# Kernel optimization log

Hardware: AMD Instinct MI355X
Metric: run time of the kernel (lower is better)

The kernel has to match this reference:

```python
import jax, jax.numpy as jnp
import numpy as np

EMBED_DIM = 1024
NUM_HEADS = 16
HEAD_DIM = EMBED_DIM // NUM_HEADS


def setup_inputs() -> dict:
    key = jax.random.key(0)
    ks = jax.random.split(key, 11)
    B, S, E = 4, 2048, EMBED_DIM
    s = 1.0 / np.sqrt(E)
    return {
        "q": jax.random.normal(ks[0], (B, S, E), jnp.float32),
        "k": jax.random.normal(ks[1], (B, S, E), jnp.float32),
        "v": jax.random.normal(ks[2], (B, S, E), jnp.float32),
        "Wq": jax.random.uniform(ks[3], (E, E), jnp.float32, -s, s),
        "bq": jax.random.uniform(ks[4], (E,), jnp.float32, -s, s),
        "Wk": jax.random.uniform(ks[5], (E, E), jnp.float32, -s, s),
        "bk": jax.random.uniform(ks[6], (E,), jnp.float32, -s, s),
        "Wv": jax.random.uniform(ks[7], (E, E), jnp.float32, -s, s),
        "bv": jax.random.uniform(ks[8], (E,), jnp.float32, -s, s),
        "Wo": jax.random.uniform(ks[9], (E, E), jnp.float32, -s, s),
        "bo": jax.random.uniform(ks[10], (E,), jnp.float32, -s, s),
    }


def _split_heads(x):
    B, S, E = x.shape
    return x.reshape(B, S, NUM_HEADS, HEAD_DIM).transpose(0, 2, 1, 3)  # [B,H,S,D]


def reference(q, k, v, Wq, bq, Wk, bk, Wv, bv, Wo, bo):
    # torch Linear: x @ W.T + b
    Q = _split_heads(q @ Wq.T + bq)
    K = _split_heads(k @ Wk.T + bk)
    V = _split_heads(v @ Wv.T + bv)
    scale = 1.0 / jnp.sqrt(jnp.float32(HEAD_DIM))
    scores = jnp.einsum("bhqd,bhkd->bhqk", Q, K) * scale  # [B,H,S,S]
    weights = jax.nn.softmax(scores, axis=-1)
    ctx = jnp.einsum("bhqk,bhkd->bhqd", weights, V)
    B, H, S, D = ctx.shape
    merged = ctx.transpose(0, 2, 1, 3).reshape(B, S, H * D)
    out = merged @ Wo.T + bo
    return out, weights
```

## Files before the change

### kernel.cpp

```cpp
#include <hip/hip_runtime.h>
#include <hip/hip_bf16.h>

typedef __bf16 bf16x8 __attribute__((ext_vector_type(8)));
typedef float f32x4 __attribute__((ext_vector_type(4)));

constexpr size_t XQ_OFF = 0;
constexpr size_t WQ_OFF = 25165824;
constexpr size_t Q_OFF  = 29360128;
constexpr size_t KK_OFF = 37748736;
constexpr size_t VT_OFF = 46137344;
constexpr size_t CTX_OFF= 54525952;

__device__ __forceinline__ void gload16(const void* g, void* s) {
    __builtin_amdgcn_global_load_lds((__attribute__((address_space(1))) void*)g,
                                     (__attribute__((address_space(3))) void*)s, 16, 0, 0);
}
#define WAIT_VM0()   asm volatile("s_waitcnt vmcnt(0)" ::: "memory")
#define WAIT_VM4()   asm volatile("s_waitcnt vmcnt(4)" ::: "memory")
#define WAIT_VM32()  asm volatile("s_waitcnt vmcnt(32)" ::: "memory")
#define WAIT_LGKM0() asm volatile("s_waitcnt lgkmcnt(0)" ::: "memory")
#define BAR()        __builtin_amdgcn_s_barrier()

__global__ __launch_bounds__(256) void convert_k(
    const float* __restrict__ q, const float* __restrict__ k, const float* __restrict__ v,
    const float* __restrict__ Wq, const float* __restrict__ Wk, const float* __restrict__ Wv,
    const float* __restrict__ Wo, __bf16* __restrict__ ws) {
    int id = blockIdx.x * 256 + threadIdx.x;
    const int NX = 1048576;
    const int NW = 131072;
    const float* src; size_t dst; int local;
    if (id < 3 * NX) {
        int z = id / NX; local = id - z * NX;
        src = (z == 0) ? q : ((z == 1) ? k : v);
        dst = XQ_OFF + (size_t)z * 8388608;
    } else {
        int i2 = id - 3 * NX;
        int z = i2 / NW; local = i2 - z * NW;
        src = (z == 0) ? Wq : ((z == 1) ? Wk : ((z == 2) ? Wv : Wo));
        dst = WQ_OFF + (size_t)z * 1048576;
    }
    const float4* s4 = (const float4*)(src + (size_t)local * 8);
    float4 a = s4[0], b = s4[1];
    bf16x8 o;
    o[0]=(__bf16)a.x; o[1]=(__bf16)a.y; o[2]=(__bf16)a.z; o[3]=(__bf16)a.w;
    o[4]=(__bf16)b.x; o[5]=(__bf16)b.y; o[6]=(__bf16)b.z; o[7]=(__bf16)b.w;
    *(bf16x8*)(ws + dst + (size_t)local * 8) = o;
}

template<int MODE>
__global__ __launch_bounds__(256) void gemm_k(
    __bf16* __restrict__ ws,
    const float* __restrict__ bq, const float* __restrict__ bk,
    const float* __restrict__ bv, const float* __restrict__ bo,
    float* __restrict__ out) {
    const int K = 1024;
    unsigned n = blockIdx.x + 64u * (blockIdx.y + 8u * blockIdx.z);
    unsigned cpx = (MODE == 0) ? 192u : 64u;
    unsigned m_ = (n & 7u) * cpx + (n >> 3);
    unsigned bx = m_ & 63u;
    unsigned rest = m_ >> 6;
    unsigned by = rest & 7u;
    unsigned bz = rest >> 3;

    int z = (int)bz;
    const __bf16* A; const __bf16* Bm; const float* bias;
    if (MODE == 0) {
        A    = ws + XQ_OFF + (size_t)z * 8388608;
        Bm   = ws + WQ_OFF + (size_t)z * 1048576;
        bias = (z == 0) ? bq : ((z == 1) ? bk : bv);
    } else {
        A    = ws + CTX_OFF;
        Bm   = ws + WQ_OFF + (size_t)3 * 1048576;
        bias = bo;
    }
    int row0 = (int)bx * 128, col0 = (int)by * 128;
    __shared__ __align__(16) __bf16 As[2][128 * 32];
    __shared__ __align__(16) __bf16 Bs[2][128 * 32];
    int t = threadIdx.x, lane = t & 63, w = t >> 6;
    int wr = w >> 1, wc = w & 1;
    f32x4 acc[4][4];
#pragma unroll
    for (int i = 0; i < 4; ++i)
#pragma unroll
        for (int j = 0; j < 4; ++j) acc[i][j] = (f32x4){0.f, 0.f, 0.f, 0.f};

    auto stage = [&](int buf, int kt) {
#pragma unroll
        for (int i = 0; i < 2; ++i) {
            int e = ((i * 4 + w) * 64 + lane) * 8;
            int r = e >> 5, c = e & 31;
            gload16(A  + (size_t)(row0 + r) * K + kt + c, &As[buf][e]);
            gload16(Bm + (size_t)(col0 + r) * K + kt + c, &Bs[buf][e]);
        }
    };

    stage(0, 0);
    int cur = 0;
    for (int kt = 0; kt < K; kt += 32) {
        bool nx = kt + 32 < K;
        if (nx) { stage(cur ^ 1, kt + 32); WAIT_VM4(); }
        else    { WAIT_VM0(); }
        BAR();
        const __bf16* Ac = As[cur];
        const __bf16* Bc = Bs[cur];
        bf16x8 af[4], bfr[4];
#pragma unroll
        for (int f = 0; f < 4; ++f) {
            af[f]  = *(const bf16x8*)&Ac[(wr * 64 + f * 16 + (lane & 15)) * 32 + (lane >> 4) * 8];
            bfr[f] = *(const bf16x8*)&Bc[(wc * 64 + f * 16 + (lane & 15)) * 32 + (lane >> 4) * 8];
        }
#pragma unroll
        for (int fr = 0; fr < 4; ++fr)
#pragma unroll
            for (int fc = 0; fc < 4; ++fc)
                acc[fr][fc] = __builtin_amdgcn_mfma_f32_16x16x32_bf16(af[fr], bfr[fc], acc[fr][fc], 0, 0, 0);
        WAIT_LGKM0();
        BAR();
        cur ^= 1;
    }

    if (MODE == 0) {
        __bf16* dqk = ws + Q_OFF + (size_t)z * 8388608;
        __bf16* dvt = ws + VT_OFF;
#pragma unroll
        for (int fr = 0; fr < 4; ++fr)
#pragma unroll
            for (int fc = 0; fc < 4; ++fc)
#pragma unroll
                for (int r = 0; r < 4; ++r) {
                    int m = row0 + wr * 64 + fr * 16 + ((lane >> 4) << 2) + r;
                    int nn = col0 + wc * 64 + fc * 16 + (lane & 15);
                    float val = acc[fr][fc][r] + bias[nn];
                    int bb = m >> 11, s = m & 2047, h = nn >> 6, d = nn & 63;
                    size_t bh = (size_t)bb * 16 + h;
                    if (z < 2) dqk[bh * 131072 + (size_t)s * 64 + d] = (__bf16)val;
                    else       dvt[bh * 131072 + (size_t)d * 2048 + s] = (__bf16)val;
                }
    } else {
#pragma unroll
        for (int fr = 0; fr < 4; ++fr)
#pragma unroll
            for (int fc = 0; fc < 4; ++fc)
#pragma unroll
                for (int r = 0; r < 4; ++r) {
                    int m = row0 + wr * 64 + fr * 16 + ((lane >> 4) << 2) + r;
                    int nn = col0 + wc * 64 + fc * 16 + (lane & 15);
                    out[(size_t)m * 1024 + nn] = acc[fr][fc][r] + bias[nn];
                }
    }
}

__global__ __launch_bounds__(512) void rowsum_k(const __bf16* __restrict__ ws,
                                                float* __restrict__ rs_out) {
    unsigned n = blockIdx.x + 8u * blockIdx.y;
    unsigned m = (n & 7u) * 64u + (n >> 3);
    int bh = (int)(m >> 3);
    int q0 = (int)(m & 7u) * 256;
    const __bf16* Qb = ws + Q_OFF  + (size_t)bh * 131072;
    const __bf16* Kb = ws + KK_OFF + (size_t)bh * 131072;
    __shared__ __align__(16) __bf16 Ks[2][64 * 64];
    int t = threadIdx.x, lane = t & 63, w = t >> 6, g = lane >> 4;
    const float SCALE = 0.125f;

    bf16x8 aq[2][2];
#pragma unroll
    for (int f = 0; f < 2; ++f) {
        int qr = q0 + w * 32 + f * 16 + (lane & 15);
        aq[f][0] = *(const bf16x8*)&Qb[(size_t)qr * 64 + g * 8];
        aq[f][1] = *(const bf16x8*)&Qb[(size_t)qr * 64 + 32 + g * 8];
    }

    { int r = t >> 3, c8 = t & 7;
      gload16(Kb + (size_t)r * 64 + ((c8 ^ (r & 7)) << 3), &Ks[0][t * 8]); }
    WAIT_VM0(); BAR();

    float rs[8] = {0.f,0.f,0.f,0.f,0.f,0.f,0.f,0.f};
    int cur = 0;
    for (int kt = 0; kt < 2048; kt += 64) {
        bool nx = kt < 1984;
        if (nx) {
            int r = t >> 3, c8 = t & 7;
            gload16(Kb + (size_t)(kt + 64 + r) * 64 + ((c8 ^ (r & 7)) << 3), &Ks[cur ^ 1][t * 8]);
        }
        const __bf16* Kc = Ks[cur];
        __builtin_amdgcn_s_setprio(1);
#pragma unroll
        for (int kc = 0; kc < 4; ++kc) {
            int krow = kc * 16 + (lane & 15);
            bf16x8 b0 = *(const bf16x8*)((const char*)Kc + krow * 128 + ((g * 16) ^ ((krow & 7) << 4)));
            bf16x8 b1 = *(const bf16x8*)((const char*)Kc + krow * 128 + (((4 + g) * 16) ^ ((krow & 7) << 4)));
#pragma unroll
            for (int f = 0; f < 2; ++f) {
                f32x4 s = (f32x4){0.f, 0.f, 0.f, 0.f};
                s = __builtin_amdgcn_mfma_f32_16x16x32_bf16(aq[f][0], b0, s, 0, 0, 0);
                s = __builtin_amdgcn_mfma_f32_16x16x32_bf16(aq[f][1], b1, s, 0, 0, 0);
#pragma unroll
                for (int r4 = 0; r4 < 4; ++r4) rs[f * 4 + r4] += __expf(s[r4] * SCALE);
            }
        }
        __builtin_amdgcn_s_setprio(0);
        WAIT_LGKM0();
        if (nx) WAIT_VM0();
        BAR();
        cur ^= 1;
    }
#pragma unroll
    for (int msk = 1; msk < 16; msk <<= 1)
#pragma unroll
        for (int i = 0; i < 8; ++i) rs[i] += __shfl_xor(rs[i], msk);
    if ((lane & 15) == 0) {
#pragma unroll
        for (int f = 0; f < 2; ++f)
#pragma unroll
            for (int r4 = 0; r4 < 4; ++r4)
                rs_out[(size_t)bh * 2048 + q0 + w * 32 + f * 16 + g * 4 + r4] = rs[f * 4 + r4];
    }
}

__global__ __launch_bounds__(512) void attnw_k(const __bf16* __restrict__ ws,
                                               const float* __restrict__ rsf,
                                               __bf16* __restrict__ wsw,
                                               float* __restrict__ wout) {
    unsigned n = blockIdx.x + 8u * blockIdx.y;
    unsigned m = (n & 7u) * 64u + (n >> 3);
    int bh = (int)(m >> 3);
    int q0 = (int)(m & 7u) * 256;

    const __bf16* Qb = ws + Q_OFF  + (size_t)bh * 131072;
    const __bf16* Kb = ws + KK_OFF + (size_t)bh * 131072;
    const __bf16* Vb = ws + VT_OFF + (size_t)bh * 131072;
    __bf16* ctx = wsw + CTX_OFF;

    int t = threadIdx.x, lane = t & 63, w = t >> 6, g = lane >> 4;
    __shared__ __align__(16) __bf16 Ps[256 * 64];
    __shared__ __align__(16) __bf16 Ks[2][64 * 64];
    __shared__ __align__(16) __bf16 Vts[2][64 * 64];
    const float SCALE = 0.125f;

    float rinv[8];
#pragma unroll
    for (int f = 0; f < 2; ++f)
#pragma unroll
        for (int r4 = 0; r4 < 4; ++r4)
            rinv[f * 4 + r4] = 1.f / rsf[(size_t)bh * 2048 + q0 + w * 32 + f * 16 + g * 4 + r4];

    bf16x8 aq[2][2];
#pragma unroll
    for (int f = 0; f < 2; ++f) {
        int qr = q0 + w * 32 + f * 16 + (lane & 15);
        aq[f][0] = *(const bf16x8*)&Qb[(size_t)qr * 64 + g * 8];
        aq[f][1] = *(const bf16x8*)&Qb[(size_t)qr * 64 + 32 + g * 8];
    }

    { int r = t >> 3, c8 = t & 7;
      gload16(Kb + (size_t)r * 64   + ((c8 ^ (r & 7)) << 3), &Ks[0][t * 8]);
      gload16(Vb + (size_t)r * 2048 + ((c8 ^ (r & 7)) << 3), &Vts[0][t * 8]); }
    WAIT_VM0(); BAR();

    f32x4 cacc[2][4];
#pragma unroll
    for (int f = 0; f < 2; ++f)
#pragma unroll
        for (int dc = 0; dc < 4; ++dc) cacc[f][dc] = (f32x4){0.f, 0.f, 0.f, 0.f};

    int cur = 0;
    for (int kt = 0; kt < 2048; kt += 64) {
        bool nx = kt < 1984;
        if (nx) {
            int r = t >> 3, c8 = t & 7;
            gload16(Kb + (size_t)(kt + 64 + r) * 64 + ((c8 ^ (r & 7)) << 3), &Ks[cur ^ 1][t * 8]);
            gload16(Vb + (size_t)r * 2048 + (kt + 64) + ((c8 ^ (r & 7)) << 3), &Vts[cur ^ 1][t * 8]);
        }
        const __bf16* Kc = Ks[cur];
        const __bf16* Vc = Vts[cur];
        __builtin_amdgcn_s_setprio(1);
#pragma unroll
        for (int kc = 0; kc < 4; ++kc) {
            int krow = kc * 16 + (lane & 15);
            bf16x8 b0 = *(const bf16x8*)((const char*)Kc + krow * 128 + ((g * 16) ^ ((krow & 7) << 4)));
            bf16x8 b1 = *(const bf16x8*)((const char*)Kc + krow * 128 + (((4 + g) * 16) ^ ((krow & 7) << 4)));
#pragma unroll
            for (int f = 0; f < 2; ++f) {
                f32x4 s = (f32x4){0.f, 0.f, 0.f, 0.f};
                s = __builtin_amdgcn_mfma_f32_16x16x32_bf16(aq[f][0], b0, s, 0, 0, 0);
                s = __builtin_amdgcn_mfma_f32_16x16x32_bf16(aq[f][1], b1, s, 0, 0, 0);
                size_t wbase = ((size_t)bh * 2048 + q0 + w * 32 + f * 16 + (g << 2)) * 2048
                               + kt + kc * 16 + (lane & 15);
#pragma unroll
                for (int r4 = 0; r4 < 4; ++r4) {
                    float e = __expf(s[r4] * SCALE) * rinv[f * 4 + r4];
                    wout[wbase + (size_t)r4 * 2048] = e;
                    int prow = w * 32 + f * 16 + (g << 2) + r4;
                    int pcol = kc * 16 + (lane & 15);
                    *(__bf16*)((char*)Ps + prow * 128 + ((pcol * 2) ^ ((prow & 7) << 4))) = (__bf16)e;
                }
            }
        }
        __builtin_amdgcn_s_setprio(0);
        WAIT_LGKM0();
        __builtin_amdgcn_sched_barrier(0);
        BAR();
        __builtin_amdgcn_s_setprio(1);
#pragma unroll
        for (int ks = 0; ks < 2; ++ks) {
            bf16x8 ap[2];
#pragma unroll
            for (int f = 0; f < 2; ++f) {
                int arow = w * 32 + f * 16 + (lane & 15);
                ap[f] = *(const bf16x8*)((const char*)Ps + arow * 128 + ((ks * 64 + g * 16) ^ ((arow & 7) << 4)));
            }
#pragma unroll
            for (int dc = 0; dc < 4; ++dc) {
                int vrow = dc * 16 + (lane & 15);
                bf16x8 bv = *(const bf16x8*)((const char*)Vc + vrow * 128 + ((ks * 64 + g * 16) ^ ((vrow & 7) << 4)));
#pragma unroll
                for (int f = 0; f < 2; ++f)
                    cacc[f][dc] = __builtin_amdgcn_mfma_f32_16x16x32_bf16(ap[f], bv, cacc[f][dc], 0, 0, 0);
            }
        }
        __builtin_amdgcn_s_setprio(0);
        WAIT_LGKM0();
        WAIT_VM32();
        BAR();
        cur ^= 1;
    }

    int bb = bh >> 4, h = bh & 15;
#pragma unroll
    for (int f = 0; f < 2; ++f)
#pragma unroll
        for (int dc = 0; dc < 4; ++dc)
#pragma unroll
            for (int r4 = 0; r4 < 4; ++r4) {
                int qg = q0 + w * 32 + f * 16 + (g << 2) + r4;
                int d = dc * 16 + (lane & 15);
                ctx[((size_t)bb * 2048 + qg) * 1024 + h * 64 + d] = (__bf16)cacc[f][dc][r4];
            }
}

extern "C" void kernel_launch(void* const* d_in, const int* in_sizes, int n_in,
                              void* d_out, int out_size, void* d_ws, size_t ws_size,
                              hipStream_t stream) {
    const float* q  = (const float*)d_in[0];
    const float* k  = (const float*)d_in[1];
    const float* v  = (const float*)d_in[2];
    const float* Wq = (const float*)d_in[3];
    const float* bq = (const float*)d_in[4];
    const float* Wk = (const float*)d_in[5];
    const float* bk = (const float*)d_in[6];
    const float* Wv = (const float*)d_in[7];
    const float* bv = (const float*)d_in[8];
    const float* Wo = (const float*)d_in[9];
    const float* bo = (const float*)d_in[10];
    __bf16* ws = (__bf16*)d_ws;
    float* out  = (float*)d_out;
    float* wout = out + 8388608;
    float* rsum = (float*)d_ws;

    convert_k<<<dim3(14336), dim3(256), 0, stream>>>(q, k, v, Wq, Wk, Wv, Wo, ws);
    gemm_k<0><<<dim3(64, 8, 3), dim3(256), 0, stream>>>(ws, bq, bk, bv, bo, out);
    rowsum_k<<<dim3(8, 64), dim3(512), 0, stream>>>(ws, rsum);
    attnw_k<<<dim3(8, 64), dim3(512), 0, stream>>>(ws, rsum, ws, wout);
    gemm_k<1><<<dim3(64, 8, 1), dim3(256), 0, stream>>>(ws, bq, bk, bv, bo, out);
}
```

Before: 558.1 us.

## Fuse rowsum into PV kernel and move weights write to separate kernel

```diff
diff --git a/kernel.cpp b/kernel.cpp
--- a/kernel.cpp
+++ b/kernel.cpp
@@ -17,7 +17,6 @@
 }
 #define WAIT_VM0()   asm volatile("s_waitcnt vmcnt(0)" ::: "memory")
 #define WAIT_VM4()   asm volatile("s_waitcnt vmcnt(4)" ::: "memory")
-#define WAIT_VM32()  asm volatile("s_waitcnt vmcnt(32)" ::: "memory")
 #define WAIT_LGKM0() asm volatile("s_waitcnt lgkmcnt(0)" ::: "memory")
 #define BAR()        __builtin_amdgcn_s_barrier()
 
@@ -150,77 +149,9 @@
     }
 }
 
-__global__ __launch_bounds__(512) void rowsum_k(const __bf16* __restrict__ ws,
-                                                float* __restrict__ rs_out) {
-    unsigned n = blockIdx.x + 8u * blockIdx.y;
-    unsigned m = (n & 7u) * 64u + (n >> 3);
-    int bh = (int)(m >> 3);
-    int q0 = (int)(m & 7u) * 256;
-    const __bf16* Qb = ws + Q_OFF  + (size_t)bh * 131072;
-    const __bf16* Kb = ws + KK_OFF + (size_t)bh * 131072;
-    __shared__ __align__(16) __bf16 Ks[2][64 * 64];
-    int t = threadIdx.x, lane = t & 63, w = t >> 6, g = lane >> 4;
-    const float SCALE = 0.125f;
-
-    bf16x8 aq[2][2];
-#pragma unroll
-    for (int f = 0; f < 2; ++f) {
-        int qr = q0 + w * 32 + f * 16 + (lane & 15);
-        aq[f][0] = *(const bf16x8*)&Qb[(size_t)qr * 64 + g * 8];
-        aq[f][1] = *(const bf16x8*)&Qb[(size_t)qr * 64 + 32 + g * 8];
-    }
-
-    { int r = t >> 3, c8 = t & 7;
-      gload16(Kb + (size_t)r * 64 + ((c8 ^ (r & 7)) << 3), &Ks[0][t * 8]); }
-    WAIT_VM0(); BAR();
-
-    float rs[8] = {0.f,0.f,0.f,0.f,0.f,0.f,0.f,0.f};
-    int cur = 0;
-    for (int kt = 0; kt < 2048; kt += 64) {
-        bool nx = kt < 1984;
-        if (nx) {
-            int r = t >> 3, c8 = t & 7;
-            gload16(Kb + (size_t)(kt + 64 + r) * 64 + ((c8 ^ (r & 7)) << 3), &Ks[cur ^ 1][t * 8]);
-        }
-        const __bf16* Kc = Ks[cur];
-        __builtin_amdgcn_s_setprio(1);
-#pragma unroll
-        for (int kc = 0; kc < 4; ++kc) {
-            int krow = kc * 16 + (lane & 15);
-            bf16x8 b0 = *(const bf16x8*)((const char*)Kc + krow * 128 + ((g * 16) ^ ((krow & 7) << 4)));
-            bf16x8 b1 = *(const bf16x8*)((const char*)Kc + krow * 128 + (((4 + g) * 16) ^ ((krow & 7) << 4)));
-#pragma unroll
-            for (int f = 0; f < 2; ++f) {
-                f32x4 s = (f32x4){0.f, 0.f, 0.f, 0.f};
-                s = __builtin_amdgcn_mfma_f32_16x16x32_bf16(aq[f][0], b0, s, 0, 0, 0);
-                s = __builtin_amdgcn_mfma_f32_16x16x32_bf16(aq[f][1], b1, s, 0, 0, 0);
-#pragma unroll
-                for (int r4 = 0; r4 < 4; ++r4) rs[f * 4 + r4] += __expf(s[r4] * SCALE);
-            }
-        }
-        __builtin_amdgcn_s_setprio(0);
-        WAIT_LGKM0();
-        if (nx) WAIT_VM0();
-        BAR();
-        cur ^= 1;
-    }
-#pragma unroll
-    for (int msk = 1; msk < 16; msk <<= 1)
-#pragma unroll
-        for (int i = 0; i < 8; ++i) rs[i] += __shfl_xor(rs[i], msk);
-    if ((lane & 15) == 0) {
-#pragma unroll
-        for (int f = 0; f < 2; ++f)
-#pragma unroll
-            for (int r4 = 0; r4 < 4; ++r4)
-                rs_out[(size_t)bh * 2048 + q0 + w * 32 + f * 16 + g * 4 + r4] = rs[f * 4 + r4];
-    }
-}
-
-__global__ __launch_bounds__(512) void attnw_k(const __bf16* __restrict__ ws,
-                                               const float* __restrict__ rsf,
-                                               __bf16* __restrict__ wsw,
-                                               float* __restrict__ wout) {
+__global__ __launch_bounds__(512) void softpv_k(const __bf16* __restrict__ ws,
+                                                float* __restrict__ rs_out,
+                                                __bf16* __restrict__ wsw) {
     unsigned n = blockIdx.x + 8u * blockIdx.y;
     unsigned m = (n & 7u) * 64u + (n >> 3);
     int bh = (int)(m >> 3);
@@ -237,13 +168,6 @@
     __shared__ __align__(16) __bf16 Vts[2][64 * 64];
     const float SCALE = 0.125f;
 
-    float rinv[8];
-#pragma unroll
-    for (int f = 0; f < 2; ++f)
-#pragma unroll
-        for (int r4 = 0; r4 < 4; ++r4)
-            rinv[f * 4 + r4] = 1.f / rsf[(size_t)bh * 2048 + q0 + w * 32 + f * 16 + g * 4 + r4];
-
     bf16x8 aq[2][2];
 #pragma unroll
     for (int f = 0; f < 2; ++f) {
@@ -262,6 +186,7 @@
     for (int f = 0; f < 2; ++f)
 #pragma unroll
         for (int dc = 0; dc < 4; ++dc) cacc[f][dc] = (f32x4){0.f, 0.f, 0.f, 0.f};
+    float rs[8] = {0.f,0.f,0.f,0.f,0.f,0.f,0.f,0.f};
 
     int cur = 0;
     for (int kt = 0; kt < 2048; kt += 64) {
@@ -284,12 +209,10 @@
                 f32x4 s = (f32x4){0.f, 0.f, 0.f, 0.f};
                 s = __builtin_amdgcn_mfma_f32_16x16x32_bf16(aq[f][0], b0, s, 0, 0, 0);
                 s = __builtin_amdgcn_mfma_f32_16x16x32_bf16(aq[f][1], b1, s, 0, 0, 0);
-                size_t wbase = ((size_t)bh * 2048 + q0 + w * 32 + f * 16 + (g << 2)) * 2048
-                               + kt + kc * 16 + (lane & 15);
 #pragma unroll
                 for (int r4 = 0; r4 < 4; ++r4) {
-                    float e = __expf(s[r4] * SCALE) * rinv[f * 4 + r4];
-                    wout[wbase + (size_t)r4 * 2048] = e;
+                    float e = __expf(s[r4] * SCALE);
+                    rs[f * 4 + r4] += e;
                     int prow = w * 32 + f * 16 + (g << 2) + r4;
                     int pcol = kc * 16 + (lane & 15);
                     *(__bf16*)((char*)Ps + prow * 128 + ((pcol * 2) ^ ((prow & 7) << 4))) = (__bf16)e;
@@ -320,9 +243,24 @@
         }
         __builtin_amdgcn_s_setprio(0);
         WAIT_LGKM0();
-        WAIT_VM32();
+        if (nx) WAIT_VM0();
         BAR();
         cur ^= 1;
+    }
+
+#pragma unroll
+    for (int msk = 1; msk < 16; msk <<= 1)
+#pragma unroll
+        for (int i = 0; i < 8; ++i) rs[i] += __shfl_xor(rs[i], msk);
+    float rinv[8];
+#pragma unroll
+    for (int i = 0; i < 8; ++i) rinv[i] = 1.f / rs[i];
+    if ((lane & 15) == 0) {
+#pragma unroll
+        for (int f = 0; f < 2; ++f)
+#pragma unroll
+            for (int r4 = 0; r4 < 4; ++r4)
+                rs_out[(size_t)bh * 2048 + q0 + w * 32 + f * 16 + g * 4 + r4] = rs[f * 4 + r4];
     }
 
     int bb = bh >> 4, h = bh & 15;
@@ -334,8 +272,64 @@
             for (int r4 = 0; r4 < 4; ++r4) {
                 int qg = q0 + w * 32 + f * 16 + (g << 2) + r4;
                 int d = dc * 16 + (lane & 15);
-                ctx[((size_t)bb * 2048 + qg) * 1024 + h * 64 + d] = (__bf16)cacc[f][dc][r4];
+                ctx[((size_t)bb * 2048 + qg) * 1024 + h * 64 + d] =
+                    (__bf16)(cacc[f][dc][r4] * rinv[f * 4 + r4]);
             }
+}
+
+__global__ __launch_bounds__(256) void weights_k(const __bf16* __restrict__ ws,
+                                                 const float* __restrict__ rsf,
+                                                 float* __restrict__ wout) {
+    unsigned n = blockIdx.x;
+    int bh = (int)((n & 7u) * 8u + ((n >> 3) & 7u));
+    int q0 = (int)(n >> 6) * 128;
+
+    const __bf16* Qb = ws + Q_OFF  + (size_t)bh * 131072;
+    const __bf16* Kb = ws + KK_OFF + (size_t)bh * 131072;
+
+    int t = threadIdx.x, lane = t & 63, w = t >> 6, g = lane >> 4;
+    int qbase = q0 + w * 32;
+    const float C = 0.125f * 1.44269504f;
+
+    bf16x8 aq[2][2];
+#pragma unroll
+    for (int f = 0; f < 2; ++f) {
+        int qr = qbase + f * 16 + (lane & 15);
+        aq[f][0] = *(const bf16x8*)&Qb[(size_t)qr * 64 + g * 8];
+        aq[f][1] = *(const bf16x8*)&Qb[(size_t)qr * 64 + 32 + g * 8];
+    }
+    float lr[2][4];
+#pragma unroll
+    for (int f = 0; f < 2; ++f)
+#pragma unroll
+        for (int r4 = 0; r4 < 4; ++r4)
+            lr[f][r4] = -__log2f(rsf[(size_t)bh * 2048 + qbase + f * 16 + g * 4 + r4]);
+
+    const __bf16* Kr = Kb + (size_t)(lane & 15) * 64;
+    bf16x8 b0 = *(const bf16x8*)&Kr[g * 8];
+    bf16x8 b1 = *(const bf16x8*)&Kr[32 + g * 8];
+
+    for (int kt = 0; kt < 2048; kt += 16) {
+        bf16x8 nb0, nb1;
+        if (kt + 16 < 2048) {
+            const __bf16* Kn = Kb + (size_t)(kt + 16 + (lane & 15)) * 64;
+            nb0 = *(const bf16x8*)&Kn[g * 8];
+            nb1 = *(const bf16x8*)&Kn[32 + g * 8];
+        }
+#pragma unroll
+        for (int f = 0; f < 2; ++f) {
+            f32x4 s = (f32x4){0.f, 0.f, 0.f, 0.f};
+            s = __builtin_amdgcn_mfma_f32_16x16x32_bf16(aq[f][0], b0, s, 0, 0, 0);
+            s = __builtin_amdgcn_mfma_f32_16x16x32_bf16(aq[f][1], b1, s, 0, 0, 0);
+            size_t wbase = ((size_t)bh * 2048 + qbase + f * 16 + (g << 2)) * 2048
+                           + kt + (lane & 15);
+#pragma unroll
+            for (int r4 = 0; r4 < 4; ++r4)
+                wout[wbase + (size_t)r4 * 2048] =
+                    __builtin_amdgcn_exp2f(__builtin_fmaf(s[r4], C, lr[f][r4]));
+        }
+        b0 = nb0; b1 = nb1;
+    }
 }
 
 extern "C" void kernel_launch(void* const* d_in, const int* in_sizes, int n_in,
@@ -359,7 +353,7 @@
 
     convert_k<<<dim3(14336), dim3(256), 0, stream>>>(q, k, v, Wq, Wk, Wv, Wo, ws);
     gemm_k<0><<<dim3(64, 8, 3), dim3(256), 0, stream>>>(ws, bq, bk, bv, bo, out);
-    rowsum_k<<<dim3(8, 64), dim3(512), 0, stream>>>(ws, rsum);
-    attnw_k<<<dim3(8, 64), dim3(512), 0, stream>>>(ws, rsum, ws, wout);
+    softpv_k<<<dim3(8, 64), dim3(512), 0, stream>>>(ws, rsum, ws);
+    weights_k<<<dim3(1024), dim3(256), 0, stream>>>(ws, rsum, wout);
     gemm_k<1><<<dim3(64, 8, 1), dim3(256), 0, stream>>>(ws, bq, bk, bv, bo, out);
 }
```

Measured after the change: 751.9 us. +34.7%, slower.

## Transpose QK MFMA, keep P in registers via shuffles, vectorize weight stores

Applied to the files above, without the earlier changes.

```diff
diff --git a/kernel.cpp b/kernel.cpp
--- a/kernel.cpp
+++ b/kernel.cpp
@@ -2,6 +2,7 @@
 #include <hip/hip_bf16.h>
 
 typedef __bf16 bf16x8 __attribute__((ext_vector_type(8)));
+typedef __bf16 bf16x4 __attribute__((ext_vector_type(4)));
 typedef float f32x4 __attribute__((ext_vector_type(4)));
 
 constexpr size_t XQ_OFF = 0;
@@ -17,7 +18,7 @@
 }
 #define WAIT_VM0()   asm volatile("s_waitcnt vmcnt(0)" ::: "memory")
 #define WAIT_VM4()   asm volatile("s_waitcnt vmcnt(4)" ::: "memory")
-#define WAIT_VM32()  asm volatile("s_waitcnt vmcnt(32)" ::: "memory")
+#define WAIT_VM8()   asm volatile("s_waitcnt vmcnt(8)" ::: "memory")
 #define WAIT_LGKM0() asm volatile("s_waitcnt lgkmcnt(0)" ::: "memory")
 #define BAR()        __builtin_amdgcn_s_barrier()
 
@@ -232,17 +233,9 @@
     __bf16* ctx = wsw + CTX_OFF;
 
     int t = threadIdx.x, lane = t & 63, w = t >> 6, g = lane >> 4;
-    __shared__ __align__(16) __bf16 Ps[256 * 64];
     __shared__ __align__(16) __bf16 Ks[2][64 * 64];
     __shared__ __align__(16) __bf16 Vts[2][64 * 64];
     const float SCALE = 0.125f;
-
-    float rinv[8];
-#pragma unroll
-    for (int f = 0; f < 2; ++f)
-#pragma unroll
-        for (int r4 = 0; r4 < 4; ++r4)
-            rinv[f * 4 + r4] = 1.f / rsf[(size_t)bh * 2048 + q0 + w * 32 + f * 16 + g * 4 + r4];
 
     bf16x8 aq[2][2];
 #pragma unroll
@@ -251,6 +244,10 @@
         aq[f][0] = *(const bf16x8*)&Qb[(size_t)qr * 64 + g * 8];
         aq[f][1] = *(const bf16x8*)&Qb[(size_t)qr * 64 + 32 + g * 8];
     }
+    float rinv[2];
+#pragma unroll
+    for (int f = 0; f < 2; ++f)
+        rinv[f] = 1.f / rsf[(size_t)bh * 2048 + q0 + w * 32 + f * 16 + (lane & 15)];
 
     { int r = t >> 3, c8 = t & 7;
       gload16(Kb + (size_t)r * 64   + ((c8 ^ (r & 7)) << 3), &Ks[0][t * 8]);
@@ -273,7 +270,8 @@
         }
         const __bf16* Kc = Ks[cur];
         const __bf16* Vc = Vts[cur];
-        __builtin_amdgcn_s_setprio(1);
+
+        int2 pk[2][4];
 #pragma unroll
         for (int kc = 0; kc < 4; ++kc) {
             int krow = kc * 16 + (lane & 15);
@@ -282,46 +280,51 @@
 #pragma unroll
             for (int f = 0; f < 2; ++f) {
                 f32x4 s = (f32x4){0.f, 0.f, 0.f, 0.f};
-                s = __builtin_amdgcn_mfma_f32_16x16x32_bf16(aq[f][0], b0, s, 0, 0, 0);
-                s = __builtin_amdgcn_mfma_f32_16x16x32_bf16(aq[f][1], b1, s, 0, 0, 0);
-                size_t wbase = ((size_t)bh * 2048 + q0 + w * 32 + f * 16 + (g << 2)) * 2048
-                               + kt + kc * 16 + (lane & 15);
-#pragma unroll
-                for (int r4 = 0; r4 < 4; ++r4) {
-                    float e = __expf(s[r4] * SCALE) * rinv[f * 4 + r4];
-                    wout[wbase + (size_t)r4 * 2048] = e;
-                    int prow = w * 32 + f * 16 + (g << 2) + r4;
-                    int pcol = kc * 16 + (lane & 15);
-                    *(__bf16*)((char*)Ps + prow * 128 + ((pcol * 2) ^ ((prow & 7) << 4))) = (__bf16)e;
+                s = __builtin_amdgcn_mfma_f32_16x16x32_bf16(b0, aq[f][0], s, 0, 0, 0);
+                s = __builtin_amdgcn_mfma_f32_16x16x32_bf16(b1, aq[f][1], s, 0, 0, 0);
+                f32x4 e4;
+#pragma unroll
+                for (int r4 = 0; r4 < 4; ++r4) e4[r4] = __expf(s[r4] * SCALE) * rinv[f];
+                float* dst = wout + ((size_t)bh * 2048 + q0 + w * 32 + f * 16 + (lane & 15)) * 2048
+                             + kt + kc * 16 + g * 4;
+                *(f32x4*)dst = e4;
+                bf16x4 p4;
+#pragma unroll
+                for (int r4 = 0; r4 < 4; ++r4) p4[r4] = (__bf16)e4[r4];
+                pk[f][kc] = __builtin_bit_cast(int2, p4);
+            }
+        }
+
+        int src0 = (lane & 15) + ((lane & 16) << 1);
+        int src1 = src0 + 16;
+        bool hi = lane >= 32;
+        __builtin_amdgcn_s_setprio(1);
+#pragma unroll
+        for (int f = 0; f < 2; ++f) {
+#pragma unroll
+            for (int ks = 0; ks < 2; ++ks) {
+                int2 A0 = pk[f][2 * ks], A1 = pk[f][2 * ks + 1];
+                int l0a = __shfl(A0.x, src0), l0b = __shfl(A1.x, src0);
+                int l1a = __shfl(A0.y, src0), l1b = __shfl(A1.y, src0);
+                int h0a = __shfl(A0.x, src1), h0b = __shfl(A1.x, src1);
+                int h1a = __shfl(A0.y, src1), h1b = __shfl(A1.y, src1);
+                int4 ai;
+                ai.x = hi ? l0b : l0a;
+                ai.y = hi ? l1b : l1a;
+                ai.z = hi ? h0b : h0a;
+                ai.w = hi ? h1b : h1a;
+                bf16x8 ap = __builtin_bit_cast(bf16x8, ai);
+#pragma unroll
+                for (int dc = 0; dc < 4; ++dc) {
+                    int vrow = dc * 16 + (lane & 15);
+                    bf16x8 bv = *(const bf16x8*)((const char*)Vc + vrow * 128 + ((ks * 64 + g * 16) ^ ((vrow & 7) << 4)));
+                    cacc[f][dc] = __builtin_amdgcn_mfma_f32_16x16x32_bf16(ap, bv, cacc[f][dc], 0, 0, 0);
                 }
             }
         }
         __builtin_amdgcn_s_setprio(0);
         WAIT_LGKM0();
-        __builtin_amdgcn_sched_barrier(0);
-        BAR();
-        __builtin_amdgcn_s_setprio(1);
-#pragma unroll
-        for (int ks = 0; ks < 2; ++ks) {
-            bf16x8 ap[2];
-#pragma unroll
-            for (int f = 0; f < 2; ++f) {
-                int arow = w * 32 + f * 16 + (lane & 15);
-                ap[f] = *(const bf16x8*)((const char*)Ps + arow * 128 + ((ks * 64 + g * 16) ^ ((arow & 7) << 4)));
-            }
-#pragma unroll
-            for (int dc = 0; dc < 4; ++dc) {
-                int vrow = dc * 16 + (lane & 15);
-                bf16x8 bv = *(const bf16x8*)((const char*)Vc + vrow * 128 + ((ks * 64 + g * 16) ^ ((vrow & 7) << 4)));
-#pragma unroll
-                for (int f = 0; f < 2; ++f)
-                    cacc[f][dc] = __builtin_amdgcn_mfma_f32_16x16x32_bf16(ap[f], bv, cacc[f][dc], 0, 0, 0);
-            }
-        }
-        __builtin_amdgcn_s_setprio(0);
-        WAIT_LGKM0();
-        WAIT_VM32();
-        BAR();
+        if (nx) { WAIT_VM8(); BAR(); }
         cur ^= 1;
     }
 
```

New measurement: 537.9 us. -3.6%, faster.
